# Kernel optimization log

Measured on AMD Instinct MI355X. Metric: run time of the kernel, lower is better.

## Reference

```python
import jax, jax.numpy as jnp
import numpy as np

B, N, K = 2, 8192, 16
D1, D2, OUT = 128, 256, 128


def setup_inputs() -> dict:
    key = jax.random.key(0)
    ks = jax.random.split(key, 6)
    return {
        "xyz1": jax.random.normal(ks[0], (B, N, 3), dtype=jnp.float32),
        "xyz2": jax.random.normal(ks[1], (B, N, 3), dtype=jnp.float32),
        "points1": jax.random.normal(ks[2], (B, N, D1), dtype=jnp.float32),
        "points2": jax.random.normal(ks[3], (B, N, D2), dtype=jnp.float32),
        # Conv1d(k=1) == pointwise linear: weight [OUT, D1+D2], bias [OUT]
        "W": jax.random.normal(ks[4], (OUT, D1 + D2), dtype=jnp.float32) / np.sqrt(D1 + D2).astype(np.float32),
        "b": jax.random.normal(ks[5], (OUT,), dtype=jnp.float32) * 0.01,
        "nsample": K,
    }


def reference(xyz1, xyz2, points1, points2, W, b, nsample):
    Bb, Nn, _ = xyz1.shape
    # squared pairwise distances, queries=xyz2, keys=xyz1 -> [B, N, N]
    d2 = (jnp.sum(xyz2 * xyz2, -1)[:, :, None]
          + jnp.sum(xyz1 * xyz1, -1)[:, None, :]
          - 2.0 * jnp.einsum('bsc,bnc->bsn', xyz2, xyz1))
    neg_vals, idx = jax.lax.top_k(-d2, nsample)          # K nearest
    dists = -neg_vals                                     # [B, N, K] sq dists
    recip = 1.0 / (dists + 1e-8)
    weight = recip / jnp.sum(recip, axis=2, keepdims=True)  # inverse-dist weights
    # gather neighbor features from points2: [B, N, K, D2]
    g = jnp.take_along_axis(points2, idx.reshape(Bb, Nn * nsample)[:, :, None], axis=1)
    g = g.reshape(Bb, Nn, nsample, -1)
    interp = jnp.sum(g * weight[..., None], axis=2)       # [B, N, D2]
    cat = jnp.concatenate([points1, interp], axis=-1)     # [B, N, D1+D2]
    # Conv1d(kernel=1) over channel dim
    return jnp.einsum('bnc,oc->bno', cat, W) + b
```

## Files before the change

kernel.cpp:

```cpp
#include <hip/hip_runtime.h>
#include <stdint.h>

#define BQ   2
#define NQ   8192
#define D1Q  128
#define D2Q  256
#define OUTQ 128
#define CATQ 384
#define KQ   16

__global__ void prep_kernel(const float* __restrict__ W, float* __restrict__ Wt,
                            const float* __restrict__ xyz1,
                            float4* __restrict__ xyz1n) {
    int flat = blockIdx.x * 256 + threadIdx.x;
    if (flat < CATQ * OUTQ) {
        int k = flat >> 7;
        int o = flat & (OUTQ - 1);
        Wt[flat] = W[o * CATQ + k];
    }
    if (flat < BQ * NQ) {
        float x = xyz1[flat * 3 + 0];
        float y = xyz1[flat * 3 + 1];
        float z = xyz1[flat * 3 + 2];
        float n;
        {
            #pragma clang fp contract(off)
            float px = x * x, py = y * y, pz = z * z;
            n = (px + py) + pz;
        }
        xyz1n[flat] = make_float4(x, y, z, n);
    }
}

__device__ __forceinline__ void fma4(float4& acc, float a, const float4& w) {
    acc.x = fmaf(a, w.x, acc.x);
    acc.y = fmaf(a, w.y, acc.y);
    acc.z = fmaf(a, w.z, acc.z);
    acc.w = fmaf(a, w.w, acc.w);
}

__device__ __forceinline__ float npy_d2(float4 pt, float qx, float qy, float qz,
                                        float s2) {
    #pragma clang fp contract(off)
    float d0  = pt.x * qx;
    float dot = fmaf(pt.y, qy, d0);
    dot       = fmaf(pt.z, qz, dot);
    float tt  = s2 + pt.w;
    return tt - 2.0f * dot;
}

__device__ __forceinline__ float red_r(float4 pt, float qx, float qy, float qz) {
    float dot = fmaf(pt.z, qz, fmaf(pt.y, qy, pt.x * qx));
    return fmaf(-2.0f, dot, pt.w);
}
#define RED_MARGIN 1e-3f

__device__ __forceinline__ uint64_t sort64(uint64_t x, int lane) {
    #pragma unroll
    for (int k = 2; k <= 64; k <<= 1) {
        #pragma unroll
        for (int j = k >> 1; j > 0; j >>= 1) {
            uint64_t p = __shfl_xor((unsigned long long)x, j, 64);
            bool keep_min = (((lane & j) == 0) == ((lane & k) == 0));
            bool pless    = p < x;
            x = (pless == keep_min) ? p : x;
        }
    }
    return x;
}

__global__ __launch_bounds__(256, 4) void fused_kernel(
        const float4* __restrict__ xyz1n, const float* __restrict__ xyz2,
        const float* __restrict__ points1, const float* __restrict__ points2,
        const float* __restrict__ Wt, const float* __restrict__ bias,
        float* __restrict__ out) {
    __shared__ __align__(16) char smem[40960];
    float4*   xyzt4 = (float4*)smem;
    uint64_t* wball = (uint64_t*)(smem + 16384);
    float*    cat   = (float*)smem;
    float*    Wl    = (float*)(smem + 24576);

    const int tid   = threadIdx.x;
    const int lane  = tid & 63;
    const int w     = tid >> 6;
    const int qbase = blockIdx.x * 16 + w * 4;
    const int b     = (blockIdx.x * 16) >> 13;

    float qx[4], qy[4], qz[4], s2[4];
    #pragma unroll
    for (int j = 0; j < 4; ++j) {
        const float* qp = xyz2 + (size_t)(qbase + j) * 3;
        qx[j] = qp[0]; qy[j] = qp[1]; qz[j] = qp[2];
        {
            #pragma clang fp contract(off)
            float px = qx[j] * qx[j], py = qy[j] * qy[j], pz = qz[j] * qz[j];
            s2[j] = (px + py) + pz;
        }
    }

    const float4* xb = xyz1n + (size_t)b * NQ;

    float mn[4];
    #pragma unroll
    for (int j = 0; j < 4; ++j) mn[j] = __uint_as_float(0x7F800000u);

    for (int tile = 0; tile < 4; ++tile) {
        __syncthreads();
        {
            const float4* s4 = xb + tile * 1024;
            #pragma unroll
            for (int v = tid; v < 1024; v += 256) xyzt4[v] = s4[v];
        }
        __syncthreads();
        #pragma unroll 4
        for (int s = 0; s < 16; ++s) {
            float4 pt = xyzt4[s * 64 + lane];
            #pragma unroll
            for (int j = 0; j < 4; ++j)
                mn[j] = fminf(mn[j], red_r(pt, qx[j], qy[j], qz[j]));
        }
    }

    float that[4];
    #pragma unroll
    for (int j = 0; j < 4; ++j) {
        float x = mn[j];
        #pragma unroll
        for (int k = 2; k <= 64; k <<= 1) {
            #pragma unroll
            for (int jj = k >> 1; jj > 0; jj >>= 1) {
                float px = __shfl_xor(x, jj, 64);
                bool keep_min = (((lane & jj) == 0) == ((lane & k) == 0));
                float mnv = fminf(x, px), mxv = fmaxf(x, px);
                x = keep_min ? mnv : mxv;
            }
        }
        that[j] = s2[j] + __shfl(x, 15, 64) + RED_MARGIN;
    }

    uint32_t cnt[4] = {0u, 0u, 0u, 0u};
    for (int tt = 0; tt < 8; ++tt) {
        const int tile = (3 + tt) & 7;
        if (tt > 0) {
            __syncthreads();
            const float4* s4 = xb + tile * 1024;
            #pragma unroll
            for (int v = tid; v < 1024; v += 256) xyzt4[v] = s4[v];
            __syncthreads();
        }
        const uint32_t base = (uint32_t)tile * 1024u;
        #pragma unroll 4
        for (int s = 0; s < 16; ++s) {
            float4 pt = xyzt4[s * 64 + lane];
            const uint32_t pidx = base + (uint32_t)(s * 64 + lane);
            #pragma unroll
            for (int j = 0; j < 4; ++j) {
                float d2 = npy_d2(pt, qx[j], qy[j], qz[j], s2[j]);
                bool  v  = (d2 <= that[j]);
                uint64_t mask = __ballot((int)v);
                if (mask != 0ull) {
                    if (v) {
                        uint32_t below = __builtin_amdgcn_mbcnt_hi(
                            (uint32_t)(mask >> 32),
                            __builtin_amdgcn_mbcnt_lo((uint32_t)mask, 0u));
                        uint32_t pos    = cnt[j] + below;
                        uint32_t bits   = __float_as_uint(d2);
                        uint32_t mapped = bits ^ (0x80000000u |
                                          (uint32_t)((int32_t)bits >> 31));
                        if (pos < 128u)
                            wball[(w * 4 + j) * 128 + pos] =
                                ((uint64_t)mapped << 32) | (uint64_t)pidx;
                    }
                    cnt[j] += (uint32_t)__popcll(mask);
                }
            }
        }
    }

    int   myidxA[4];
    float mywgtA[4];
    #pragma unroll
    for (int j = 0; j < 4; ++j) {
        const uint64_t* wb = wball + (size_t)(w * 4 + j) * 128;
        const uint32_t c = cnt[j];
        uint64_t mykey;
        if (c <= 64u) {
            uint64_t k0 = (lane < (int)c) ? wb[lane] : ~0ull;
            mykey = sort64(k0, lane);
        } else {
            uint32_t cc = c > 128u ? 128u : c;
            uint64_t k0 = wb[lane];
            uint64_t k1 = (lane + 64 < (int)cc) ? wb[lane + 64] : ~0ull;
            k0 = sort64(k0, lane);
            k1 = sort64(k1, lane);
            uint64_t t1 = __shfl((unsigned long long)k1, lane & 15, 64);
            uint64_t km = (lane < 16) ? k0 : ((lane < 32) ? t1 : ~0ull);
            mykey = sort64(km, lane);
        }
        uint32_t mhi   = (uint32_t)(mykey >> 32);
        uint32_t rbits = (mhi & 0x80000000u) ? (mhi ^ 0x80000000u) : ~mhi;
        float    d2w   = __uint_as_float(rbits);
        myidxA[j] = (int)(uint32_t)(mykey & 0xFFFFFFFFull);
        float recip = (lane < KQ) ? (1.0f / (d2w + 1e-8f)) : 0.0f;
        float tot = recip;
        #pragma unroll
        for (int sh = 1; sh < 16; sh <<= 1) tot += __shfl_xor(tot, sh, 64);
        mywgtA[j] = recip / tot;
    }

    __syncthreads();

    const float* p2b = points2 + (size_t)b * NQ * D2Q;
    #pragma unroll
    for (int j = 0; j < 4; ++j) {
        const int qi = w * 4 + j;
        if (lane < 32) {
            float4 p = ((const float4*)(points1 + (size_t)(qbase + j) * D1Q))[lane];
            *(float4*)&cat[qi * CATQ + lane * 4] = p;
        }
        float4 acc = make_float4(0.f, 0.f, 0.f, 0.f);
        #pragma unroll
        for (int k = 0; k < KQ; ++k) {
            int   kk = __builtin_amdgcn_readlane(myidxA[j], k);
            float wk = __uint_as_float((uint32_t)__builtin_amdgcn_readlane(
                           (int)__float_as_uint(mywgtA[j]), k));
            float4 row = ((const float4*)(p2b + (size_t)kk * D2Q))[lane];
            acc.x = fmaf(wk, row.x, acc.x);
            acc.y = fmaf(wk, row.y, acc.y);
            acc.z = fmaf(wk, row.z, acc.z);
            acc.w = fmaf(wk, row.w, acc.w);
        }
        *(float4*)&cat[qi * CATQ + D1Q + lane * 4] = acc;
    }
    __syncthreads();

    const int rg = tid >> 5;
    const int o0 = (tid & 31) * 4;
    float4 acc0 = make_float4(0.f, 0.f, 0.f, 0.f);
    float4 acc1 = make_float4(0.f, 0.f, 0.f, 0.f);

    for (int c = 0; c < 12; ++c) {
        if (c) __syncthreads();
        {
            const float4* src = (const float4*)(Wt + (size_t)c * 32 * OUTQ);
            #pragma unroll
            for (int i = 0; i < 4; ++i)
                ((float4*)Wl)[tid + 256 * i] = src[tid + 256 * i];
        }
        __syncthreads();

        const int kb = c * 32;
        #pragma unroll
        for (int k4 = 0; k4 < 8; ++k4) {
            const float* wb = Wl + (k4 * 4) * OUTQ + o0;
            float4 w0 = *(const float4*)(wb + 0 * OUTQ);
            float4 w1 = *(const float4*)(wb + 1 * OUTQ);
            float4 w2 = *(const float4*)(wb + 2 * OUTQ);
            float4 w3 = *(const float4*)(wb + 3 * OUTQ);
            float4 a0 = *(const float4*)&cat[(rg * 2 + 0) * CATQ + kb + k4 * 4];
            float4 a1 = *(const float4*)&cat[(rg * 2 + 1) * CATQ + kb + k4 * 4];
            fma4(acc0, a0.x, w0); fma4(acc0, a0.y, w1);
            fma4(acc0, a0.z, w2); fma4(acc0, a0.w, w3);
            fma4(acc1, a1.x, w0); fma4(acc1, a1.y, w1);
            fma4(acc1, a1.z, w2); fma4(acc1, a1.w, w3);
        }
    }

    {
        float4 bv = *(const float4*)(bias + o0);
        acc0.x += bv.x; acc0.y += bv.y; acc0.z += bv.z; acc0.w += bv.w;
        acc1.x += bv.x; acc1.y += bv.y; acc1.z += bv.z; acc1.w += bv.w;
        const int q0 = blockIdx.x * 16 + rg * 2;
        *(float4*)&out[(size_t)(q0 + 0) * OUTQ + o0] = acc0;
        *(float4*)&out[(size_t)(q0 + 1) * OUTQ + o0] = acc1;
    }
}

extern "C" void kernel_launch(void* const* d_in, const int* in_sizes, int n_in,
                              void* d_out, int out_size, void* d_ws, size_t ws_size,
                              hipStream_t stream) {
    const float* xyz1    = (const float*)d_in[0];
    const float* xyz2    = (const float*)d_in[1];
    const float* points1 = (const float*)d_in[2];
    const float* points2 = (const float*)d_in[3];
    const float* W       = (const float*)d_in[4];
    const float* bias    = (const float*)d_in[5];

    float* wsf  = (float*)d_ws;
    float* Wt   = wsf;
    float4* xyz1n = (float4*)(wsf + 49152);

    prep_kernel<<<192, 256, 0, stream>>>(W, Wt, xyz1, xyz1n);
    fused_kernel<<<(BQ * NQ) / 16, 256, 0, stream>>>(
        xyz1n, xyz2, points1, points2, Wt, bias, (float*)d_out);
}
```

Baseline: 179.9 us.

## Compute pointwise linear layer with split-bf16 MFMA instead of scalar FMA

```diff
diff --git a/kernel.cpp b/kernel.cpp
--- a/kernel.cpp
+++ b/kernel.cpp
@@ -9,14 +9,34 @@
 #define CATQ 384
 #define KQ   16
 
-__global__ void prep_kernel(const float* __restrict__ W, float* __restrict__ Wt,
+__device__ __forceinline__ ushort f2bf(float f) {
+    uint32_t u = __float_as_uint(f);
+    return (ushort)((u + 0x7FFFu + ((u >> 16) & 1u)) >> 16);
+}
+__device__ __forceinline__ float bf2f(ushort h) {
+    return __uint_as_float((uint32_t)h << 16);
+}
+
+typedef __attribute__((ext_vector_type(8))) short short8v;
+typedef __attribute__((ext_vector_type(4))) float f32x4v;
+
+__global__ void prep_kernel(const float* __restrict__ W,
+                            ushort* __restrict__ Wfh, ushort* __restrict__ Wfl,
                             const float* __restrict__ xyz1,
                             float4* __restrict__ xyz1n) {
     int flat = blockIdx.x * 256 + threadIdx.x;
     if (flat < CATQ * OUTQ) {
-        int k = flat >> 7;
-        int o = flat & (OUTQ - 1);
-        Wt[flat] = W[o * CATQ + k];
+        int r    = flat & 7;
+        int lane = (flat >> 3) & 63;
+        int ctk  = flat >> 9;
+        int ct   = ctk & 7;
+        int kt   = ctk >> 3;
+        int o = ct * 16 + (lane & 15);
+        int k = kt * 32 + (lane >> 4) * 8 + r;
+        float v  = W[o * CATQ + k];
+        ushort h = f2bf(v);
+        Wfh[flat] = h;
+        Wfl[flat] = f2bf(v - bf2f(h));
     }
     if (flat < BQ * NQ) {
         float x = xyz1[flat * 3 + 0];
@@ -69,16 +89,16 @@
     return x;
 }
 
-__global__ __launch_bounds__(256, 4) void fused_kernel(
+__global__ __launch_bounds__(256, 5) void fused_kernel(
         const float4* __restrict__ xyz1n, const float* __restrict__ xyz2,
         const float* __restrict__ points1, const float* __restrict__ points2,
-        const float* __restrict__ Wt, const float* __restrict__ bias,
-        float* __restrict__ out) {
-    __shared__ __align__(16) char smem[40960];
+        const ushort* __restrict__ Wfh, const ushort* __restrict__ Wfl,
+        const float* __restrict__ bias, float* __restrict__ out) {
+    __shared__ __align__(16) char smem[32768];
     float4*   xyzt4 = (float4*)smem;
     uint64_t* wball = (uint64_t*)(smem + 16384);
-    float*    cat   = (float*)smem;
-    float*    Wl    = (float*)(smem + 24576);
+    ushort*   cat_h = (ushort*)smem;
+    ushort*   cat_l = (ushort*)(smem + 12544);
 
     const int tid   = threadIdx.x;
     const int lane  = tid & 63;
@@ -216,7 +236,13 @@
         const int qi = w * 4 + j;
         if (lane < 32) {
             float4 p = ((const float4*)(points1 + (size_t)(qbase + j) * D1Q))[lane];
-            *(float4*)&cat[qi * CATQ + lane * 4] = p;
+            ushort4 hv, lv;
+            hv.x = f2bf(p.x); lv.x = f2bf(p.x - bf2f(hv.x));
+            hv.y = f2bf(p.y); lv.y = f2bf(p.y - bf2f(hv.y));
+            hv.z = f2bf(p.z); lv.z = f2bf(p.z - bf2f(hv.z));
+            hv.w = f2bf(p.w); lv.w = f2bf(p.w - bf2f(hv.w));
+            *(ushort4*)&cat_h[qi * 392 + lane * 4] = hv;
+            *(ushort4*)&cat_l[qi * 392 + lane * 4] = lv;
         }
         float4 acc = make_float4(0.f, 0.f, 0.f, 0.f);
         #pragma unroll
@@ -230,49 +256,50 @@
             acc.z = fmaf(wk, row.z, acc.z);
             acc.w = fmaf(wk, row.w, acc.w);
         }
-        *(float4*)&cat[qi * CATQ + D1Q + lane * 4] = acc;
+        {
+            ushort4 hv, lv;
+            hv.x = f2bf(acc.x); lv.x = f2bf(acc.x - bf2f(hv.x));
+            hv.y = f2bf(acc.y); lv.y = f2bf(acc.y - bf2f(hv.y));
+            hv.z = f2bf(acc.z); lv.z = f2bf(acc.z - bf2f(hv.z));
+            hv.w = f2bf(acc.w); lv.w = f2bf(acc.w - bf2f(hv.w));
+            *(ushort4*)&cat_h[qi * 392 + D1Q + lane * 4] = hv;
+            *(ushort4*)&cat_l[qi * 392 + D1Q + lane * 4] = lv;
+        }
     }
     __syncthreads();
 
-    const int rg = tid >> 5;
-    const int o0 = (tid & 31) * 4;
-    float4 acc0 = make_float4(0.f, 0.f, 0.f, 0.f);
-    float4 acc1 = make_float4(0.f, 0.f, 0.f, 0.f);
-
-    for (int c = 0; c < 12; ++c) {
-        if (c) __syncthreads();
-        {
-            const float4* src = (const float4*)(Wt + (size_t)c * 32 * OUTQ);
-            #pragma unroll
-            for (int i = 0; i < 4; ++i)
-                ((float4*)Wl)[tid + 256 * i] = src[tid + 256 * i];
-        }
-        __syncthreads();
-
-        const int kb = c * 32;
-        #pragma unroll
-        for (int k4 = 0; k4 < 8; ++k4) {
-            const float* wb = Wl + (k4 * 4) * OUTQ + o0;
-            float4 w0 = *(const float4*)(wb + 0 * OUTQ);
-            float4 w1 = *(const float4*)(wb + 1 * OUTQ);
-            float4 w2 = *(const float4*)(wb + 2 * OUTQ);
-            float4 w3 = *(const float4*)(wb + 3 * OUTQ);
-            float4 a0 = *(const float4*)&cat[(rg * 2 + 0) * CATQ + kb + k4 * 4];
-            float4 a1 = *(const float4*)&cat[(rg * 2 + 1) * CATQ + kb + k4 * 4];
-            fma4(acc0, a0.x, w0); fma4(acc0, a0.y, w1);
-            fma4(acc0, a0.z, w2); fma4(acc0, a0.w, w3);
-            fma4(acc1, a1.x, w0); fma4(acc1, a1.y, w1);
-            fma4(acc1, a1.z, w2); fma4(acc1, a1.w, w3);
-        }
-    }
-
     {
-        float4 bv = *(const float4*)(bias + o0);
-        acc0.x += bv.x; acc0.y += bv.y; acc0.z += bv.z; acc0.w += bv.w;
-        acc1.x += bv.x; acc1.y += bv.y; acc1.z += bv.z; acc1.w += bv.w;
-        const int q0 = blockIdx.x * 16 + rg * 2;
-        *(float4*)&out[(size_t)(q0 + 0) * OUTQ + o0] = acc0;
-        *(float4*)&out[(size_t)(q0 + 1) * OUTQ + o0] = acc1;
+        const int arow = lane & 15;
+        const int koff = (lane >> 4) * 8;
+        const int ct0  = w * 2;
+        f32x4v acc0 = {0.f, 0.f, 0.f, 0.f};
+        f32x4v acc1 = {0.f, 0.f, 0.f, 0.f};
+        #pragma unroll 4
+        for (int kt = 0; kt < 12; ++kt) {
+            short8v ah = *(const short8v*)&cat_h[arow * 392 + kt * 32 + koff];
+            short8v al = *(const short8v*)&cat_l[arow * 392 + kt * 32 + koff];
+            const ushort* bhp = Wfh + ((size_t)(kt * 8 + ct0) * 64 + lane) * 8;
+            const ushort* blp = Wfl + ((size_t)(kt * 8 + ct0) * 64 + lane) * 8;
+            short8v bh0 = *(const short8v*)bhp;
+            short8v bl0 = *(const short8v*)blp;
+            short8v bh1 = *(const short8v*)(bhp + 512);
+            short8v bl1 = *(const short8v*)(blp + 512);
+            acc0 = __builtin_amdgcn_mfma_f32_16x16x32_bf16(ah, bh0, acc0, 0, 0, 0);
+            acc0 = __builtin_amdgcn_mfma_f32_16x16x32_bf16(al, bh0, acc0, 0, 0, 0);
+            acc0 = __builtin_amdgcn_mfma_f32_16x16x32_bf16(ah, bl0, acc0, 0, 0, 0);
+            acc1 = __builtin_amdgcn_mfma_f32_16x16x32_bf16(ah, bh1, acc1, 0, 0, 0);
+            acc1 = __builtin_amdgcn_mfma_f32_16x16x32_bf16(al, bh1, acc1, 0, 0, 0);
+            acc1 = __builtin_amdgcn_mfma_f32_16x16x32_bf16(ah, bl1, acc1, 0, 0, 0);
+        }
+        const int col0 = ct0 * 16 + (lane & 15);
+        const int row0 = blockIdx.x * 16 + (lane >> 4) * 4;
+        const float bv0 = bias[col0];
+        const float bv1 = bias[col0 + 16];
+        #pragma unroll
+        for (int r = 0; r < 4; ++r) {
+            out[(size_t)(row0 + r) * OUTQ + col0]      = acc0[r] + bv0;
+            out[(size_t)(row0 + r) * OUTQ + col0 + 16] = acc1[r] + bv1;
+        }
     }
 }
 
@@ -286,11 +313,11 @@
     const float* W       = (const float*)d_in[4];
     const float* bias    = (const float*)d_in[5];
 
-    float* wsf  = (float*)d_ws;
-    float* Wt   = wsf;
-    float4* xyz1n = (float4*)(wsf + 49152);
-
-    prep_kernel<<<192, 256, 0, stream>>>(W, Wt, xyz1, xyz1n);
+    ushort* Wfh   = (ushort*)d_ws;
+    ushort* Wfl   = (ushort*)((char*)d_ws + 98304);
+    float4* xyz1n = (float4*)((char*)d_ws + 196608);
+
+    prep_kernel<<<192, 256, 0, stream>>>(W, Wfh, Wfl, xyz1, xyz1n);
     fused_kernel<<<(BQ * NQ) / 16, 256, 0, stream>>>(
-        xyz1n, xyz2, points1, points2, Wt, bias, (float*)d_out);
-}
+        xyz1n, xyz2, points1, points2, Wfh, Wfl, bias, (float*)d_out);
+}
```

Result: faster. 162.9 us (-9.4%).
